# Kernel tuning notes

Hardware: AMD Instinct MI355X
Metric: run time of the kernel (lower is better)

Reference implementation:

```python
import jax, jax.numpy as jnp
import numpy as np

B, T, D = 128, 2048, 256
LAMDA = 0.5


def setup_inputs() -> dict:
    key = jax.random.key(0)
    ks = jax.random.split(key, 8)
    return {
        "sentiment": jax.random.normal(ks[0], (B, D), jnp.float32),
        "aspect": jax.random.normal(ks[1], (B, D), jnp.float32),
        "sentiment_memory": jax.random.normal(ks[2], (B, T, D), jnp.float32),
        "aspect_memory": jax.random.normal(ks[3], (B, T, D), jnp.float32),
        "mask": jnp.ones((B, T), jnp.float32),
        # MultiplicativeAttention params: rand(D,D)*0.2-0.1, bias zeros(1)
        "W_mul": jax.random.uniform(ks[4], (D, D), jnp.float32) * 0.2 - 0.1,
        "b_mul": jnp.zeros((1,), jnp.float32),
        # AdditiveAttention: Linear(2D, 1) -> weight vector [2D], bias [1]
        "w_ss": jax.random.normal(ks[5], (2 * D,), jnp.float32) * 0.02,
        "b_ss": jnp.zeros((1,), jnp.float32),
        "w_sa": jax.random.normal(ks[6], (2 * D,), jnp.float32) * 0.02,
        "b_sa": jnp.zeros((1,), jnp.float32),
    }


def _masked_norm(scores, mask):
    # exp(scores - max) * mask, normalized (matches torch branch exactly)
    s = scores - jnp.max(scores, axis=1, keepdims=True)
    e = jnp.exp(s) * mask
    return e / jnp.sum(e, axis=1, keepdims=True)


def _additive_attn(query, key_mem, w, b, mask):
    # Linear([key; query_repeated]) == key @ w_k + query @ w_q + b
    d = query.shape[-1]
    scores = key_mem @ w[:d] + (query @ w[d:])[:, None] + b[0]  # [B,T]
    return _masked_norm(scores, mask)


def reference(sentiment, aspect, sentiment_memory, aspect_memory, mask,
              W_mul, b_mul, w_ss, b_ss, w_sa, b_sa):
    # Multiplicative attention over aspect_memory (no mask -> plain softmax)
    mids = aspect @ W_mul.T                                        # W @ q, [B,D]
    a_scores = jnp.tanh(jnp.einsum('btd,bd->bt', aspect_memory, mids) + b_mul[0])
    aspect_attn = jax.nn.softmax(a_scores, axis=1)                 # [B,T]
    new_aspect = jnp.einsum('bt,btd->bd', aspect_attn, aspect_memory)  # [B,D]

    ss_attn = _additive_attn(sentiment, sentiment_memory, w_ss, b_ss, mask)
    sa_attn = _additive_attn(new_aspect, sentiment_memory, w_sa, b_sa, mask)
    s_attn = (1.0 - LAMDA) * ss_attn + LAMDA * sa_attn             # [B,T]

    sentiment_out = jnp.einsum('bt,btd->bd', s_attn, sentiment_memory)[:, None, :]  # [B,1,D]
    aspect_out = aspect + new_aspect                                # [B,D]
    return sentiment_out, aspect_out
```

## Files before the change

kernel.cpp:

```cpp
#include <hip/hip_runtime.h>
#include <math.h>

#define BB 128
#define TT 2048
#define DD 256
#define SPLIT 8
#define ROWS_PER_BLOCK (TT / SPLIT)
#define WAVES 4
#define G 16
#define RPB 4
#define NB 16

#define WS_MIDS 0
#define WS_P1ACC (WS_MIDS + BB * DD)
#define WS_P1SUM (WS_P1ACC + BB * SPLIT * DD)
#define WS_P2ACC_SS (WS_P1SUM + BB * SPLIT)
#define WS_P2ACC_SA (WS_P2ACC_SS + BB * SPLIT * DD)
#define WS_P2SUM_SS (WS_P2ACC_SA + BB * SPLIT * DD)
#define WS_P2SUM_SA (WS_P2SUM_SS + BB * SPLIT)

__device__ __forceinline__ float dot4(const float4& a, const float4& b) {
    return a.x * b.x + a.y * b.y + a.z * b.z + a.w * b.w;
}

__device__ __forceinline__ float tanh_fast(float x) {
    float ax = fabsf(x);
    float t = __expf(-2.0f * ax);
    float th = (1.0f - t) / (1.0f + t);
    return copysignf(th, x);
}

__device__ __forceinline__ float4 shfl_xor4(float4 v, int off) {
    float4 r;
    r.x = __shfl_xor(v.x, off, 64);
    r.y = __shfl_xor(v.y, off, 64);
    r.z = __shfl_xor(v.z, off, 64);
    r.w = __shfl_xor(v.w, off, 64);
    return r;
}

__global__ __launch_bounds__(DD) void mids_kernel(
    const float* __restrict__ aspect, const float* __restrict__ W,
    float* __restrict__ ws)
{
    const int b = blockIdx.x;
    const int i = threadIdx.x;
    __shared__ float a[DD];
    a[i] = aspect[b * DD + i];
    __syncthreads();
    const float4* wrow = (const float4*)(W + (size_t)i * DD);
    float acc = 0.f;
    #pragma unroll 8
    for (int j4 = 0; j4 < DD / 4; ++j4) {
        float4 w4 = wrow[j4];
        acc += a[4 * j4 + 0] * w4.x + a[4 * j4 + 1] * w4.y +
               a[4 * j4 + 2] * w4.z + a[4 * j4 + 3] * w4.w;
    }
    ws[WS_MIDS + b * DD + i] = acc;
}

__global__ __launch_bounds__(256) void pass_kernel(
    const float* __restrict__ smem_g, const float* __restrict__ amem_g,
    const float* __restrict__ mask, const float* __restrict__ w_ss,
    const float* __restrict__ w_sa, const float* __restrict__ b_mul,
    float* __restrict__ ws)
{
    const int s = blockIdx.x;
    const int b = blockIdx.y;
    const int tid = threadIdx.x;
    const int wave = tid >> 6;
    const int lane = tid & 63;
    const int g = lane >> 4;
    const int c = lane & 15;
    const int t0 = s * ROWS_PER_BLOCK + wave * (RPB * NB);

    __shared__ __align__(16) float lds_acc[2 * WAVES * DD];
    __shared__ float lds_sum[2 * WAVES];

    if (blockIdx.z == 0) {
        float4 m4[4];
        #pragma unroll
        for (int j = 0; j < 4; ++j)
            m4[j] = *(const float4*)(ws + WS_MIDS + b * DD + j * 64 + c * 4);
        const float bm = b_mul[0];
        const float* base = amem_g + ((size_t)b * TT + t0 + g) * DD + c * 4;

        float4 cur[4], nxt[4];
        #pragma unroll
        for (int j = 0; j < 4; ++j)
            cur[j] = *(const float4*)(base + j * 64);

        float4 acc[4];
        #pragma unroll
        for (int j = 0; j < 4; ++j) acc[j] = make_float4(0.f, 0.f, 0.f, 0.f);
        float lsum = 0.f;

        #pragma unroll
        for (int i = 0; i < NB; ++i) {
            if (i + 1 < NB) {
                #pragma unroll
                for (int j = 0; j < 4; ++j)
                    nxt[j] = *(const float4*)(base + (size_t)(i + 1) * RPB * DD + j * 64);
            }
            float d = 0.f;
            #pragma unroll
            for (int j = 0; j < 4; ++j) d += dot4(cur[j], m4[j]);
            #pragma unroll
            for (int off = 1; off < G; off <<= 1)
                d += __shfl_xor(d, off, 64);
            float e = __expf(tanh_fast(d + bm));
            lsum += e;
            #pragma unroll
            for (int j = 0; j < 4; ++j) {
                acc[j].x += e * cur[j].x; acc[j].y += e * cur[j].y;
                acc[j].z += e * cur[j].z; acc[j].w += e * cur[j].w;
            }
            #pragma unroll
            for (int j = 0; j < 4; ++j) cur[j] = nxt[j];
        }
        #pragma unroll
        for (int j = 0; j < 4; ++j) {
            float4 o = shfl_xor4(acc[j], 16);
            acc[j].x += o.x; acc[j].y += o.y; acc[j].z += o.z; acc[j].w += o.w;
            o = shfl_xor4(acc[j], 32);
            acc[j].x += o.x; acc[j].y += o.y; acc[j].z += o.z; acc[j].w += o.w;
        }
        lsum += __shfl_xor(lsum, 16, 64);
        lsum += __shfl_xor(lsum, 32, 64);
        if (g == 0) {
            #pragma unroll
            for (int j = 0; j < 4; ++j)
                *(float4*)(lds_acc + wave * DD + j * 64 + c * 4) = acc[j];
        }
        if (lane == 0) lds_sum[wave] = lsum;
        __syncthreads();
        float tot = lds_acc[0 * DD + tid] + lds_acc[1 * DD + tid] +
                    lds_acc[2 * DD + tid] + lds_acc[3 * DD + tid];
        ws[WS_P1ACC + (size_t)(b * SPLIT + s) * DD + tid] = tot;
        if (tid == 0)
            ws[WS_P1SUM + b * SPLIT + s] =
                lds_sum[0] + lds_sum[1] + lds_sum[2] + lds_sum[3];
    } else {
        float4 wss4[4], wsa4[4];
        #pragma unroll
        for (int j = 0; j < 4; ++j) {
            wss4[j] = *(const float4*)(w_ss + j * 64 + c * 4);
            wsa4[j] = *(const float4*)(w_sa + j * 64 + c * 4);
        }
        const float* base = smem_g + ((size_t)b * TT + t0 + g) * DD + c * 4;
        const float* mrow = mask + (size_t)b * TT + t0;

        float4 cur[4], nxt[4];
        #pragma unroll
        for (int j = 0; j < 4; ++j)
            cur[j] = *(const float4*)(base + j * 64);

        float4 accss[4], accsa[4];
        #pragma unroll
        for (int j = 0; j < 4; ++j) {
            accss[j] = make_float4(0.f, 0.f, 0.f, 0.f);
            accsa[j] = make_float4(0.f, 0.f, 0.f, 0.f);
        }
        float lss = 0.f, lsa = 0.f;

        #pragma unroll
        for (int i = 0; i < NB; ++i) {
            if (i + 1 < NB) {
                #pragma unroll
                for (int j = 0; j < 4; ++j)
                    nxt[j] = *(const float4*)(base + (size_t)(i + 1) * RPB * DD + j * 64);
            }
            float dss = 0.f, dsa = 0.f;
            #pragma unroll
            for (int j = 0; j < 4; ++j) {
                dss += dot4(cur[j], wss4[j]);
                dsa += dot4(cur[j], wsa4[j]);
            }
            #pragma unroll
            for (int off = 1; off < G; off <<= 1) {
                dss += __shfl_xor(dss, off, 64);
                dsa += __shfl_xor(dsa, off, 64);
            }
            float m = mrow[i * RPB + g];
            float ess = __expf(dss) * m;
            float esa = __expf(dsa) * m;
            lss += ess;
            lsa += esa;
            #pragma unroll
            for (int j = 0; j < 4; ++j) {
                accss[j].x += ess * cur[j].x; accss[j].y += ess * cur[j].y;
                accss[j].z += ess * cur[j].z; accss[j].w += ess * cur[j].w;
                accsa[j].x += esa * cur[j].x; accsa[j].y += esa * cur[j].y;
                accsa[j].z += esa * cur[j].z; accsa[j].w += esa * cur[j].w;
            }
            #pragma unroll
            for (int j = 0; j < 4; ++j) cur[j] = nxt[j];
        }
        #pragma unroll
        for (int j = 0; j < 4; ++j) {
            float4 o = shfl_xor4(accss[j], 16);
            accss[j].x += o.x; accss[j].y += o.y; accss[j].z += o.z; accss[j].w += o.w;
            o = shfl_xor4(accss[j], 32);
            accss[j].x += o.x; accss[j].y += o.y; accss[j].z += o.z; accss[j].w += o.w;
            o = shfl_xor4(accsa[j], 16);
            accsa[j].x += o.x; accsa[j].y += o.y; accsa[j].z += o.z; accsa[j].w += o.w;
            o = shfl_xor4(accsa[j], 32);
            accsa[j].x += o.x; accsa[j].y += o.y; accsa[j].z += o.z; accsa[j].w += o.w;
        }
        lss += __shfl_xor(lss, 16, 64);
        lss += __shfl_xor(lss, 32, 64);
        lsa += __shfl_xor(lsa, 16, 64);
        lsa += __shfl_xor(lsa, 32, 64);
        if (g == 0) {
            #pragma unroll
            for (int j = 0; j < 4; ++j) {
                *(float4*)(lds_acc + wave * DD + j * 64 + c * 4) = accss[j];
                *(float4*)(lds_acc + (WAVES + wave) * DD + j * 64 + c * 4) = accsa[j];
            }
        }
        if (lane == 0) {
            lds_sum[wave] = lss;
            lds_sum[WAVES + wave] = lsa;
        }
        __syncthreads();
        float tot_ss = lds_acc[0 * DD + tid] + lds_acc[1 * DD + tid] +
                       lds_acc[2 * DD + tid] + lds_acc[3 * DD + tid];
        float tot_sa = lds_acc[(WAVES + 0) * DD + tid] + lds_acc[(WAVES + 1) * DD + tid] +
                       lds_acc[(WAVES + 2) * DD + tid] + lds_acc[(WAVES + 3) * DD + tid];
        ws[WS_P2ACC_SS + (size_t)(b * SPLIT + s) * DD + tid] = tot_ss;
        ws[WS_P2ACC_SA + (size_t)(b * SPLIT + s) * DD + tid] = tot_sa;
        if (tid == 0) {
            ws[WS_P2SUM_SS + b * SPLIT + s] =
                lds_sum[0] + lds_sum[1] + lds_sum[2] + lds_sum[3];
            ws[WS_P2SUM_SA + b * SPLIT + s] =
                lds_sum[4] + lds_sum[5] + lds_sum[6] + lds_sum[7];
        }
    }
}

__global__ __launch_bounds__(DD) void combine_kernel(
    const float* __restrict__ aspect, const float* __restrict__ ws,
    float* __restrict__ out)
{
    const int b = blockIdx.x;
    const int d = threadIdx.x;
    if (blockIdx.y == 0) {
        float acc = 0.f, l = 0.f;
        #pragma unroll
        for (int s = 0; s < SPLIT; ++s)
            acc += ws[WS_P1ACC + (size_t)(b * SPLIT + s) * DD + d];
        #pragma unroll
        for (int s = 0; s < SPLIT; ++s)
            l += ws[WS_P1SUM + b * SPLIT + s];
        out[BB * DD + b * DD + d] = aspect[b * DD + d] + acc / l;
    } else {
        float ass = 0.f, asa = 0.f, lss = 0.f, lsa = 0.f;
        #pragma unroll
        for (int s = 0; s < SPLIT; ++s) {
            ass += ws[WS_P2ACC_SS + (size_t)(b * SPLIT + s) * DD + d];
            asa += ws[WS_P2ACC_SA + (size_t)(b * SPLIT + s) * DD + d];
        }
        #pragma unroll
        for (int s = 0; s < SPLIT; ++s) {
            lss += ws[WS_P2SUM_SS + b * SPLIT + s];
            lsa += ws[WS_P2SUM_SA + b * SPLIT + s];
        }
        out[b * DD + d] = 0.5f * (ass / lss) + 0.5f * (asa / lsa);
    }
}

extern "C" void kernel_launch(void* const* d_in, const int* in_sizes, int n_in,
                              void* d_out, int out_size, void* d_ws, size_t ws_size,
                              hipStream_t stream) {
    (void)in_sizes; (void)n_in; (void)out_size; (void)ws_size;
    const float* aspect = (const float*)d_in[1];
    const float* smem   = (const float*)d_in[2];
    const float* amem   = (const float*)d_in[3];
    const float* mask   = (const float*)d_in[4];
    const float* W_mul  = (const float*)d_in[5];
    const float* b_mul  = (const float*)d_in[6];
    const float* w_ss   = (const float*)d_in[7];
    const float* w_sa   = (const float*)d_in[9];
    float* out = (float*)d_out;
    float* ws  = (float*)d_ws;

    mids_kernel<<<BB, DD, 0, stream>>>(aspect, W_mul, ws);
    pass_kernel<<<dim3(SPLIT, BB, 2), 256, 0, stream>>>(
        smem, amem, mask, w_ss, w_sa, b_mul, ws);
    combine_kernel<<<dim3(BB, 2), DD, 0, stream>>>(aspect, ws, out);
}
```

Baseline: 552.7 us.

## Split fused pass into separate sentiment and aspect kernels with 32-lane row groups

Replaces the single z-dispatched pass kernel with two specialised kernels, each with its own launch bounds and occupancy hint (6 and 4 blocks per CU), so the lighter aspect path no longer carries the register and LDS footprint of the sentiment path. Each row is now handled by 32 lanes holding 2 float4s instead of 16 lanes holding 4, which cuts registers per thread and drops one cross-group shuffle stage but adds one more step to the in-row dot-product reduction. The two kernels now run back to back on one stream instead of sharing a grid, so the aspect and sentiment streams can no longer overlap.

```diff
diff --git a/kernel.cpp b/kernel.cpp
--- a/kernel.cpp
+++ b/kernel.cpp
@@ -7,9 +7,7 @@
 #define SPLIT 8
 #define ROWS_PER_BLOCK (TT / SPLIT)
 #define WAVES 4
-#define G 16
-#define RPB 4
-#define NB 16
+#define NBATCH 32
 
 #define WS_MIDS 0
 #define WS_P1ACC (WS_MIDS + BB * DD)
@@ -59,10 +57,8 @@
     ws[WS_MIDS + b * DD + i] = acc;
 }
 
-__global__ __launch_bounds__(256) void pass_kernel(
-    const float* __restrict__ smem_g, const float* __restrict__ amem_g,
-    const float* __restrict__ mask, const float* __restrict__ w_ss,
-    const float* __restrict__ w_sa, const float* __restrict__ b_mul,
+__global__ __launch_bounds__(256, 6) void aspect_pass(
+    const float* __restrict__ amem_g, const float* __restrict__ b_mul,
     float* __restrict__ ws)
 {
     const int s = blockIdx.x;
@@ -70,171 +66,166 @@
     const int tid = threadIdx.x;
     const int wave = tid >> 6;
     const int lane = tid & 63;
-    const int g = lane >> 4;
-    const int c = lane & 15;
-    const int t0 = s * ROWS_PER_BLOCK + wave * (RPB * NB);
+    const int g = lane >> 5;
+    const int c = lane & 31;
+    const int t0 = s * ROWS_PER_BLOCK + wave * 64;
+
+    __shared__ __align__(16) float lds_acc[WAVES * DD];
+    __shared__ float lds_sum[WAVES];
+
+    float4 m4[2];
+    #pragma unroll
+    for (int j = 0; j < 2; ++j)
+        m4[j] = *(const float4*)(ws + WS_MIDS + b * DD + j * 128 + c * 4);
+    const float bm = b_mul[0];
+    const float* base = amem_g + ((size_t)b * TT + t0 + g) * DD + c * 4;
+
+    float4 cur[2], nxt[2];
+    #pragma unroll
+    for (int j = 0; j < 2; ++j) cur[j] = *(const float4*)(base + j * 128);
+    float4 acc[2];
+    acc[0] = make_float4(0.f, 0.f, 0.f, 0.f);
+    acc[1] = make_float4(0.f, 0.f, 0.f, 0.f);
+    float lsum = 0.f;
+
+    #pragma unroll
+    for (int i = 0; i < NBATCH; ++i) {
+        if (i + 1 < NBATCH) {
+            #pragma unroll
+            for (int j = 0; j < 2; ++j)
+                nxt[j] = *(const float4*)(base + (size_t)(i + 1) * 2 * DD + j * 128);
+        }
+        float d = dot4(cur[0], m4[0]) + dot4(cur[1], m4[1]);
+        #pragma unroll
+        for (int off = 1; off < 32; off <<= 1)
+            d += __shfl_xor(d, off, 64);
+        float e = __expf(tanh_fast(d + bm));
+        lsum += e;
+        #pragma unroll
+        for (int j = 0; j < 2; ++j) {
+            acc[j].x += e * cur[j].x; acc[j].y += e * cur[j].y;
+            acc[j].z += e * cur[j].z; acc[j].w += e * cur[j].w;
+        }
+        cur[0] = nxt[0]; cur[1] = nxt[1];
+    }
+    #pragma unroll
+    for (int j = 0; j < 2; ++j) {
+        float4 o = shfl_xor4(acc[j], 32);
+        acc[j].x += o.x; acc[j].y += o.y; acc[j].z += o.z; acc[j].w += o.w;
+    }
+    lsum += __shfl_xor(lsum, 32, 64);
+    if (g == 0) {
+        #pragma unroll
+        for (int j = 0; j < 2; ++j)
+            *(float4*)(lds_acc + wave * DD + j * 128 + c * 4) = acc[j];
+    }
+    if (lane == 0) lds_sum[wave] = lsum;
+    __syncthreads();
+    float tot = lds_acc[0 * DD + tid] + lds_acc[1 * DD + tid] +
+                lds_acc[2 * DD + tid] + lds_acc[3 * DD + tid];
+    ws[WS_P1ACC + (size_t)(b * SPLIT + s) * DD + tid] = tot;
+    if (tid == 0)
+        ws[WS_P1SUM + b * SPLIT + s] =
+            lds_sum[0] + lds_sum[1] + lds_sum[2] + lds_sum[3];
+}
+
+__global__ __launch_bounds__(256, 4) void sent_pass(
+    const float* __restrict__ smem_g, const float* __restrict__ mask,
+    const float* __restrict__ w_ss, const float* __restrict__ w_sa,
+    float* __restrict__ ws)
+{
+    const int s = blockIdx.x;
+    const int b = blockIdx.y;
+    const int tid = threadIdx.x;
+    const int wave = tid >> 6;
+    const int lane = tid & 63;
+    const int g = lane >> 5;
+    const int c = lane & 31;
+    const int t0 = s * ROWS_PER_BLOCK + wave * 64;
 
     __shared__ __align__(16) float lds_acc[2 * WAVES * DD];
     __shared__ float lds_sum[2 * WAVES];
 
-    if (blockIdx.z == 0) {
-        float4 m4[4];
-        #pragma unroll
-        for (int j = 0; j < 4; ++j)
-            m4[j] = *(const float4*)(ws + WS_MIDS + b * DD + j * 64 + c * 4);
-        const float bm = b_mul[0];
-        const float* base = amem_g + ((size_t)b * TT + t0 + g) * DD + c * 4;
-
-        float4 cur[4], nxt[4];
-        #pragma unroll
-        for (int j = 0; j < 4; ++j)
-            cur[j] = *(const float4*)(base + j * 64);
-
-        float4 acc[4];
-        #pragma unroll
-        for (int j = 0; j < 4; ++j) acc[j] = make_float4(0.f, 0.f, 0.f, 0.f);
-        float lsum = 0.f;
-
-        #pragma unroll
-        for (int i = 0; i < NB; ++i) {
-            if (i + 1 < NB) {
-                #pragma unroll
-                for (int j = 0; j < 4; ++j)
-                    nxt[j] = *(const float4*)(base + (size_t)(i + 1) * RPB * DD + j * 64);
-            }
-            float d = 0.f;
+    float4 wss4[2], wsa4[2];
+    #pragma unroll
+    for (int j = 0; j < 2; ++j) {
+        wss4[j] = *(const float4*)(w_ss + j * 128 + c * 4);
+        wsa4[j] = *(const float4*)(w_sa + j * 128 + c * 4);
+    }
+    const float* base = smem_g + ((size_t)b * TT + t0 + g) * DD + c * 4;
+    const float* mrow = mask + (size_t)b * TT + t0;
+
+    float4 cur[2], nxt[2];
+    #pragma unroll
+    for (int j = 0; j < 2; ++j) cur[j] = *(const float4*)(base + j * 128);
+    float4 accss[2], accsa[2];
+    #pragma unroll
+    for (int j = 0; j < 2; ++j) {
+        accss[j] = make_float4(0.f, 0.f, 0.f, 0.f);
+        accsa[j] = make_float4(0.f, 0.f, 0.f, 0.f);
+    }
+    float lss = 0.f, lsa = 0.f;
+
+    #pragma unroll
+    for (int i = 0; i < NBATCH; ++i) {
+        if (i + 1 < NBATCH) {
             #pragma unroll
-            for (int j = 0; j < 4; ++j) d += dot4(cur[j], m4[j]);
-            #pragma unroll
-            for (int off = 1; off < G; off <<= 1)
-                d += __shfl_xor(d, off, 64);
-            float e = __expf(tanh_fast(d + bm));
-            lsum += e;
-            #pragma unroll
-            for (int j = 0; j < 4; ++j) {
-                acc[j].x += e * cur[j].x; acc[j].y += e * cur[j].y;
-                acc[j].z += e * cur[j].z; acc[j].w += e * cur[j].w;
-            }
-            #pragma unroll
-            for (int j = 0; j < 4; ++j) cur[j] = nxt[j];
-        }
-        #pragma unroll
-        for (int j = 0; j < 4; ++j) {
-            float4 o = shfl_xor4(acc[j], 16);
-            acc[j].x += o.x; acc[j].y += o.y; acc[j].z += o.z; acc[j].w += o.w;
-            o = shfl_xor4(acc[j], 32);
-            acc[j].x += o.x; acc[j].y += o.y; acc[j].z += o.z; acc[j].w += o.w;
-        }
-        lsum += __shfl_xor(lsum, 16, 64);
-        lsum += __shfl_xor(lsum, 32, 64);
-        if (g == 0) {
-            #pragma unroll
-            for (int j = 0; j < 4; ++j)
-                *(float4*)(lds_acc + wave * DD + j * 64 + c * 4) = acc[j];
-        }
-        if (lane == 0) lds_sum[wave] = lsum;
-        __syncthreads();
-        float tot = lds_acc[0 * DD + tid] + lds_acc[1 * DD + tid] +
-                    lds_acc[2 * DD + tid] + lds_acc[3 * DD + tid];
-        ws[WS_P1ACC + (size_t)(b * SPLIT + s) * DD + tid] = tot;
-        if (tid == 0)
-            ws[WS_P1SUM + b * SPLIT + s] =
-                lds_sum[0] + lds_sum[1] + lds_sum[2] + lds_sum[3];
-    } else {
-        float4 wss4[4], wsa4[4];
-        #pragma unroll
-        for (int j = 0; j < 4; ++j) {
-            wss4[j] = *(const float4*)(w_ss + j * 64 + c * 4);
-            wsa4[j] = *(const float4*)(w_sa + j * 64 + c * 4);
-        }
-        const float* base = smem_g + ((size_t)b * TT + t0 + g) * DD + c * 4;
-        const float* mrow = mask + (size_t)b * TT + t0;
-
-        float4 cur[4], nxt[4];
-        #pragma unroll
-        for (int j = 0; j < 4; ++j)
-            cur[j] = *(const float4*)(base + j * 64);
-
-        float4 accss[4], accsa[4];
-        #pragma unroll
-        for (int j = 0; j < 4; ++j) {
-            accss[j] = make_float4(0.f, 0.f, 0.f, 0.f);
-            accsa[j] = make_float4(0.f, 0.f, 0.f, 0.f);
-        }
-        float lss = 0.f, lsa = 0.f;
-
-        #pragma unroll
-        for (int i = 0; i < NB; ++i) {
-            if (i + 1 < NB) {
-                #pragma unroll
-                for (int j = 0; j < 4; ++j)
-                    nxt[j] = *(const float4*)(base + (size_t)(i + 1) * RPB * DD + j * 64);
-            }
-            float dss = 0.f, dsa = 0.f;
-            #pragma unroll
-            for (int j = 0; j < 4; ++j) {
-                dss += dot4(cur[j], wss4[j]);
-                dsa += dot4(cur[j], wsa4[j]);
-            }
-            #pragma unroll
-            for (int off = 1; off < G; off <<= 1) {
-                dss += __shfl_xor(dss, off, 64);
-                dsa += __shfl_xor(dsa, off, 64);
-            }
-            float m = mrow[i * RPB + g];
-            float ess = __expf(dss) * m;
-            float esa = __expf(dsa) * m;
-            lss += ess;
-            lsa += esa;
-            #pragma unroll
-            for (int j = 0; j < 4; ++j) {
-                accss[j].x += ess * cur[j].x; accss[j].y += ess * cur[j].y;
-                accss[j].z += ess * cur[j].z; accss[j].w += ess * cur[j].w;
-                accsa[j].x += esa * cur[j].x; accsa[j].y += esa * cur[j].y;
-                accsa[j].z += esa * cur[j].z; accsa[j].w += esa * cur[j].w;
-            }
-            #pragma unroll
-            for (int j = 0; j < 4; ++j) cur[j] = nxt[j];
-        }
-        #pragma unroll
-        for (int j = 0; j < 4; ++j) {
-            float4 o = shfl_xor4(accss[j], 16);
-            accss[j].x += o.x; accss[j].y += o.y; accss[j].z += o.z; accss[j].w += o.w;
-            o = shfl_xor4(accss[j], 32);
-            accss[j].x += o.x; accss[j].y += o.y; accss[j].z += o.z; accss[j].w += o.w;
-            o = shfl_xor4(accsa[j], 16);
-            accsa[j].x += o.x; accsa[j].y += o.y; accsa[j].z += o.z; accsa[j].w += o.w;
-            o = shfl_xor4(accsa[j], 32);
-            accsa[j].x += o.x; accsa[j].y += o.y; accsa[j].z += o.z; accsa[j].w += o.w;
-        }
-        lss += __shfl_xor(lss, 16, 64);
-        lss += __shfl_xor(lss, 32, 64);
-        lsa += __shfl_xor(lsa, 16, 64);
-        lsa += __shfl_xor(lsa, 32, 64);
-        if (g == 0) {
-            #pragma unroll
-            for (int j = 0; j < 4; ++j) {
-                *(float4*)(lds_acc + wave * DD + j * 64 + c * 4) = accss[j];
-                *(float4*)(lds_acc + (WAVES + wave) * DD + j * 64 + c * 4) = accsa[j];
-            }
-        }
-        if (lane == 0) {
-            lds_sum[wave] = lss;
-            lds_sum[WAVES + wave] = lsa;
-        }
-        __syncthreads();
-        float tot_ss = lds_acc[0 * DD + tid] + lds_acc[1 * DD + tid] +
-                       lds_acc[2 * DD + tid] + lds_acc[3 * DD + tid];
-        float tot_sa = lds_acc[(WAVES + 0) * DD + tid] + lds_acc[(WAVES + 1) * DD + tid] +
-                       lds_acc[(WAVES + 2) * DD + tid] + lds_acc[(WAVES + 3) * DD + tid];
-        ws[WS_P2ACC_SS + (size_t)(b * SPLIT + s) * DD + tid] = tot_ss;
-        ws[WS_P2ACC_SA + (size_t)(b * SPLIT + s) * DD + tid] = tot_sa;
-        if (tid == 0) {
-            ws[WS_P2SUM_SS + b * SPLIT + s] =
-                lds_sum[0] + lds_sum[1] + lds_sum[2] + lds_sum[3];
-            ws[WS_P2SUM_SA + b * SPLIT + s] =
-                lds_sum[4] + lds_sum[5] + lds_sum[6] + lds_sum[7];
-        }
+            for (int j = 0; j < 2; ++j)
+                nxt[j] = *(const float4*)(base + (size_t)(i + 1) * 2 * DD + j * 128);
+        }
+        float dss = dot4(cur[0], wss4[0]) + dot4(cur[1], wss4[1]);
+        float dsa = dot4(cur[0], wsa4[0]) + dot4(cur[1], wsa4[1]);
+        #pragma unroll
+        for (int off = 1; off < 32; off <<= 1) {
+            dss += __shfl_xor(dss, off, 64);
+            dsa += __shfl_xor(dsa, off, 64);
+        }
+        float m = mrow[i * 2 + g];
+        float ess = __expf(dss) * m;
+        float esa = __expf(dsa) * m;
+        lss += ess;
+        lsa += esa;
+        #pragma unroll
+        for (int j = 0; j < 2; ++j) {
+            accss[j].x += ess * cur[j].x; accss[j].y += ess * cur[j].y;
+            accss[j].z += ess * cur[j].z; accss[j].w += ess * cur[j].w;
+            accsa[j].x += esa * cur[j].x; accsa[j].y += esa * cur[j].y;
+            accsa[j].z += esa * cur[j].z; accsa[j].w += esa * cur[j].w;
+        }
+        cur[0] = nxt[0]; cur[1] = nxt[1];
+    }
+    #pragma unroll
+    for (int j = 0; j < 2; ++j) {
+        float4 o = shfl_xor4(accss[j], 32);
+        accss[j].x += o.x; accss[j].y += o.y; accss[j].z += o.z; accss[j].w += o.w;
+        o = shfl_xor4(accsa[j], 32);
+        accsa[j].x += o.x; accsa[j].y += o.y; accsa[j].z += o.z; accsa[j].w += o.w;
+    }
+    lss += __shfl_xor(lss, 32, 64);
+    lsa += __shfl_xor(lsa, 32, 64);
+    if (g == 0) {
+        #pragma unroll
+        for (int j = 0; j < 2; ++j) {
+            *(float4*)(lds_acc + wave * DD + j * 128 + c * 4) = accss[j];
+            *(float4*)(lds_acc + (WAVES + wave) * DD + j * 128 + c * 4) = accsa[j];
+        }
+    }
+    if (lane == 0) {
+        lds_sum[wave] = lss;
+        lds_sum[WAVES + wave] = lsa;
+    }
+    __syncthreads();
+    float tot_ss = lds_acc[0 * DD + tid] + lds_acc[1 * DD + tid] +
+                   lds_acc[2 * DD + tid] + lds_acc[3 * DD + tid];
+    float tot_sa = lds_acc[(WAVES + 0) * DD + tid] + lds_acc[(WAVES + 1) * DD + tid] +
+                   lds_acc[(WAVES + 2) * DD + tid] + lds_acc[(WAVES + 3) * DD + tid];
+    ws[WS_P2ACC_SS + (size_t)(b * SPLIT + s) * DD + tid] = tot_ss;
+    ws[WS_P2ACC_SA + (size_t)(b * SPLIT + s) * DD + tid] = tot_sa;
+    if (tid == 0) {
+        ws[WS_P2SUM_SS + b * SPLIT + s] =
+            lds_sum[0] + lds_sum[1] + lds_sum[2] + lds_sum[3];
+        ws[WS_P2SUM_SA + b * SPLIT + s] =
+            lds_sum[4] + lds_sum[5] + lds_sum[6] + lds_sum[7];
     }
 }
 
@@ -285,7 +276,7 @@
     float* ws  = (float*)d_ws;
 
     mids_kernel<<<BB, DD, 0, stream>>>(aspect, W_mul, ws);
-    pass_kernel<<<dim3(SPLIT, BB, 2), 256, 0, stream>>>(
-        smem, amem, mask, w_ss, w_sa, b_mul, ws);
+    sent_pass<<<dim3(SPLIT, BB), 256, 0, stream>>>(smem, mask, w_ss, w_sa, ws);
+    aspect_pass<<<dim3(SPLIT, BB), 256, 0, stream>>>(amem, b_mul, ws);
     combine_kernel<<<dim3(BB, 2), DD, 0, stream>>>(aspect, ws, out);
 }
```

Measured after the change: 689.9 us. 1.25x slower.
